# Performance work log

Measured on AMD Instinct MI355X. Metric: run time of the kernel, lower is better.

## Reference

```python
import jax, jax.numpy as jnp
import numpy as np

B, N, D, F = 16, 64, 32, 32  # batch, nodes, node_dim, nb_features


def setup_inputs() -> dict:
    key = jax.random.key(0)
    k1, k2, k3, k4, k5 = jax.random.split(key, 5)
    nodes = jax.random.normal(k1, (B, N, D), dtype=jnp.float32)
    edges = jax.random.normal(k2, (B, N * N, F), dtype=jnp.float32)
    mask = jax.random.randint(k3, (B, N * N, 1), 0, 2).astype(jnp.float32)
    # Linear(nb_features -> node_dim**2) params, torch-style fan-in scaling
    lim = 1.0 / np.sqrt(F)
    W = jax.random.uniform(k4, (D * D, F), dtype=jnp.float32, minval=-lim, maxval=lim)
    b = jax.random.uniform(k5, (D * D,), dtype=jnp.float32, minval=-lim, maxval=lim)
    return {"nodes": nodes, "edges": edges, "mask": mask, "W": W, "b": b}


def reference(nodes, edges, mask, W, b):
    Bn, Nn, d = nodes.shape
    # ECC weight generation: per-edge d x d matrix from edge features
    A = jax.nn.relu(jnp.einsum('bef,gf->beg', edges, W) + b)      # [B, N*N, d*d]
    A = A.reshape(Bn, Nn, Nn, d, d)                               # [B, i, j, d, d]
    # node_j tiling: flat edge index i*N+j pairs with source node j
    messages = jnp.einsum('bijde,bje->bijd', A, nodes)            # [B, i, j, d]
    masked = messages * mask.reshape(Bn, Nn, Nn, 1)
    agg_m = jnp.sum(masked, axis=2)                               # [B, N, d]
    return agg_m
```

## Files before the change

kernel.cpp:

```cpp
#include <hip/hip_runtime.h>
#include <hip/hip_bf16.h>


#define B_ 16
#define N_ 64
#define D_ 32
#define F_ 32
#define NP 33

typedef __attribute__((ext_vector_type(8))) short bf16x8;
typedef __attribute__((ext_vector_type(4))) float f32x4;

__device__ __forceinline__ short f2bf(float x) {
    unsigned u = __builtin_bit_cast(unsigned, x);
    u += 0x7fffu + ((u >> 16) & 1u);
    return (short)(u >> 16);
}

__global__ __launch_bounds__(256) void ecc_fused_kernel(
    const float* __restrict__ nodes,
    const float* __restrict__ edges,
    const float* __restrict__ mask,
    const float* __restrict__ W,
    const float* __restrict__ bias,
    float* __restrict__ out)
{
    __shared__ short wlds[512 * F_];
    __shared__ float nmask[N_ * NP];
    __shared__ float blds[D_ * D_];

    const int tid  = threadIdx.x;
    const int lane = tid & 63;
    const int wv   = tid >> 6;
    const int col  = lane & 15;
    const int grp  = lane >> 4;
    const int bi   = blockIdx.x;
    const int b    = bi >> 6;
    const int i    = bi & 63;
    const int f0   = grp * 8;

    {
        const int j  = tid >> 2;
        const int c0 = (tid & 3) * 8;
        const float mk = mask[b * (N_ * N_) + i * N_ + j];
        const float* np = nodes + (b * N_ + j) * D_ + c0;
        f32x4 v0 = *(const f32x4*)np;
        f32x4 v1 = *(const f32x4*)(np + 4);
        float* dst = &nmask[j * NP + c0];
        dst[0] = v0[0] * mk; dst[1] = v0[1] * mk;
        dst[2] = v0[2] * mk; dst[3] = v0[3] * mk;
        dst[4] = v1[0] * mk; dst[5] = v1[1] * mk;
        dst[6] = v1[2] * mk; dst[7] = v1[3] * mk;
        *(f32x4*)(blds + tid * 4) = *(const f32x4*)(bias + tid * 4);
    }

    const float* eb = edges + (b * (N_ * N_) + i * N_) * F_;
    bf16x8 bfrag[4];
#pragma unroll
    for (int jt = 0; jt < 4; ++jt) {
        const float* s = eb + (jt * 16 + col) * F_ + f0;
        f32x4 e0 = *(const f32x4*)s;
        f32x4 e1 = *(const f32x4*)(s + 4);
        bf16x8 t;
        t[0] = f2bf(e0[0]); t[1] = f2bf(e0[1]); t[2] = f2bf(e0[2]); t[3] = f2bf(e0[3]);
        t[4] = f2bf(e1[0]); t[5] = f2bf(e1[1]); t[6] = f2bf(e1[2]); t[7] = f2bf(e1[3]);
        bfrag[jt] = t;
    }

    float acc[8] = {0.f, 0.f, 0.f, 0.f, 0.f, 0.f, 0.f, 0.f};

#pragma unroll 1
    for (int par = 0; par < 2; ++par) {
        __syncthreads();

#pragma unroll 2
        for (int k = 0; k < 8; ++k) {
            const int lidx = k * 2048 + tid * 8;
            const int lr   = lidx >> 5;
            const int fo   = lidx & 31;
            const int g    = (((lr >> 4) * 2 + par) * 16) + (lr & 15);
            const float* s = W + g * F_ + fo;
            f32x4 a0 = *(const f32x4*)s;
            f32x4 a1 = *(const f32x4*)(s + 4);
            bf16x8 t;
            t[0] = f2bf(a0[0]); t[1] = f2bf(a0[1]);
            t[2] = f2bf(a0[2]); t[3] = f2bf(a0[3]);
            t[4] = f2bf(a1[0]); t[5] = f2bf(a1[1]);
            t[6] = f2bf(a1[2]); t[7] = f2bf(a1[3]);
            *(bf16x8*)(wlds + lidx) = t;
        }
        __syncthreads();

        float nd[4][4];
#pragma unroll
        for (int jt = 0; jt < 4; ++jt) {
            const float* n = &nmask[(jt * 16 + col) * NP + par * 16 + grp * 4];
            nd[jt][0] = n[0]; nd[jt][1] = n[1];
            nd[jt][2] = n[2]; nd[jt][3] = n[3];
        }

#pragma unroll 1
        for (int g8 = 0; g8 < 8; ++g8) {
            const int gt   = wv * 16 + g8 * 2 + par;
            const int lrow = (wv * 8 + g8) * 16 + col;
            bf16x8 afrag = *(const bf16x8*)(wlds + lrow * F_ + f0);
            f32x4 bfr = *(const f32x4*)(blds + gt * 16 + grp * 4);

#pragma unroll
            for (int jt = 0; jt < 4; ++jt) {
                f32x4 c = __builtin_amdgcn_mfma_f32_16x16x32_bf16(afrag, bfrag[jt], bfr, 0, 0, 0);
                float s = fmaxf(c[0], 0.f) * nd[jt][0];
                s += fmaxf(c[1], 0.f) * nd[jt][1];
                s += fmaxf(c[2], 0.f) * nd[jt][2];
                s += fmaxf(c[3], 0.f) * nd[jt][3];
                acc[g8] += s;
            }
        }
    }

#pragma unroll
    for (int dl = 0; dl < 8; ++dl) {
        float v = acc[dl];
#pragma unroll
        for (int off = 32; off > 0; off >>= 1) v += __shfl_xor(v, off, 64);
        acc[dl] = v;
    }

    if (lane == 0) {
        float* op = out + (b * N_ + i) * D_ + wv * 8;
#pragma unroll
        for (int dl = 0; dl < 8; ++dl) op[dl] = acc[dl];
    }
}

extern "C" void kernel_launch(void* const* d_in, const int* in_sizes, int n_in,
                              void* d_out, int out_size, void* d_ws, size_t ws_size,
                              hipStream_t stream) {
    const float* nodes = (const float*)d_in[0];
    const float* edges = (const float*)d_in[1];
    const float* mask  = (const float*)d_in[2];
    const float* W     = (const float*)d_in[3];
    const float* bias  = (const float*)d_in[4];
    float* outp        = (float*)d_out;

    ecc_fused_kernel<<<dim3(B_ * N_), dim3(256), 0, stream>>>(
        nodes, edges, mask, W, bias, outp);
}
```

Measured before the change: 86.75 us.

## Compact masked edges per row and load full swizzled W tile once

Builds a compacted list of unmasked source nodes per (batch, row) with a ballot and popcount, then gathers only those edges and node vectors and skips MFMA tiles past the active count. The whole bf16 W matrix is staged into LDS once with an XOR swizzle instead of twice per parity pass, which removes a barrier pair and reduces bank conflicts. This uses 64KB of LDS, which may lower occupancy, and adds a data-dependent branch on the tile count. Since the mask is random, about half the MFMA work is skipped.

Measured after the change: 92.72 us. +6.9%, slower.

```diff
diff --git a/kernel.cpp b/kernel.cpp
--- a/kernel.cpp
+++ b/kernel.cpp
@@ -25,9 +25,11 @@
     const float* __restrict__ bias,
     float* __restrict__ out)
 {
-    __shared__ short wlds[512 * F_];
+    __shared__ short wlds[D_ * D_ * F_];
     __shared__ float nmask[N_ * NP];
     __shared__ float blds[D_ * D_];
+    __shared__ int   jlist[N_];
+    __shared__ int   jcnt;
 
     const int tid  = threadIdx.x;
     const int lane = tid & 63;
@@ -39,81 +41,102 @@
     const int i    = bi & 63;
     const int f0   = grp * 8;
 
+    *(f32x4*)(blds + tid * 4) = *(const f32x4*)(bias + tid * 4);
+
+    if (tid < 64) {
+        const float mk = mask[b * (N_ * N_) + i * N_ + tid];
+        jlist[tid] = 0;
+        const unsigned long long act = __ballot(mk != 0.0f);
+        if (tid == 0) jcnt = (int)__popcll(act);
+        if (mk != 0.0f) {
+            const int pos = (int)__popcll(act & ((1ull << tid) - 1ull));
+            jlist[pos] = tid;
+        }
+    }
+
+#pragma unroll 1
+    for (int k = 0; k < 16; ++k) {
+        const int lidx = k * 2048 + tid * 8;
+        const int lr   = lidx >> 5;
+        const int fo   = lidx & 31;
+        const float* s = W + lr * F_ + fo;
+        f32x4 a0 = *(const f32x4*)s;
+        f32x4 a1 = *(const f32x4*)(s + 4);
+        bf16x8 t;
+        t[0] = f2bf(a0[0]); t[1] = f2bf(a0[1]);
+        t[2] = f2bf(a0[2]); t[3] = f2bf(a0[3]);
+        t[4] = f2bf(a1[0]); t[5] = f2bf(a1[1]);
+        t[6] = f2bf(a1[2]); t[7] = f2bf(a1[3]);
+        *(bf16x8*)(wlds + lr * F_ + (fo ^ ((lr & 3) * 8))) = t;
+    }
+    __syncthreads();
+
     {
-        const int j  = tid >> 2;
-        const int c0 = (tid & 3) * 8;
-        const float mk = mask[b * (N_ * N_) + i * N_ + j];
-        const float* np = nodes + (b * N_ + j) * D_ + c0;
-        f32x4 v0 = *(const f32x4*)np;
-        f32x4 v1 = *(const f32x4*)(np + 4);
-        float* dst = &nmask[j * NP + c0];
-        dst[0] = v0[0] * mk; dst[1] = v0[1] * mk;
-        dst[2] = v0[2] * mk; dst[3] = v0[3] * mk;
-        dst[4] = v1[0] * mk; dst[5] = v1[1] * mk;
-        dst[6] = v1[2] * mk; dst[7] = v1[3] * mk;
-        *(f32x4*)(blds + tid * 4) = *(const f32x4*)(bias + tid * 4);
+        const int slot = tid >> 2;
+        const int c0   = (tid & 3) * 8;
+        f32x4 v0 = {0.f, 0.f, 0.f, 0.f}, v1 = {0.f, 0.f, 0.f, 0.f};
+        if (slot < jcnt) {
+            const float* np = nodes + (b * N_ + jlist[slot]) * D_ + c0;
+            v0 = *(const f32x4*)np;
+            v1 = *(const f32x4*)(np + 4);
+        }
+        float* dst = &nmask[slot * NP + c0];
+        dst[0] = v0[0]; dst[1] = v0[1]; dst[2] = v0[2]; dst[3] = v0[3];
+        dst[4] = v1[0]; dst[5] = v1[1]; dst[6] = v1[2]; dst[7] = v1[3];
     }
+
+    const int NT = (jcnt + 15) >> 4;
 
     const float* eb = edges + (b * (N_ * N_) + i * N_) * F_;
     bf16x8 bfrag[4];
 #pragma unroll
     for (int jt = 0; jt < 4; ++jt) {
-        const float* s = eb + (jt * 16 + col) * F_ + f0;
-        f32x4 e0 = *(const f32x4*)s;
-        f32x4 e1 = *(const f32x4*)(s + 4);
-        bf16x8 t;
-        t[0] = f2bf(e0[0]); t[1] = f2bf(e0[1]); t[2] = f2bf(e0[2]); t[3] = f2bf(e0[3]);
-        t[4] = f2bf(e1[0]); t[5] = f2bf(e1[1]); t[6] = f2bf(e1[2]); t[7] = f2bf(e1[3]);
-        bfrag[jt] = t;
+        if (jt < NT) {
+            const int j = jlist[jt * 16 + col];
+            const float* s = eb + j * F_ + f0;
+            f32x4 e0 = *(const f32x4*)s;
+            f32x4 e1 = *(const f32x4*)(s + 4);
+            bf16x8 t;
+            t[0] = f2bf(e0[0]); t[1] = f2bf(e0[1]);
+            t[2] = f2bf(e0[2]); t[3] = f2bf(e0[3]);
+            t[4] = f2bf(e1[0]); t[5] = f2bf(e1[1]);
+            t[6] = f2bf(e1[2]); t[7] = f2bf(e1[3]);
+            bfrag[jt] = t;
+        }
     }
+    __syncthreads();
 
     float acc[8] = {0.f, 0.f, 0.f, 0.f, 0.f, 0.f, 0.f, 0.f};
 
 #pragma unroll 1
     for (int par = 0; par < 2; ++par) {
-        __syncthreads();
-
-#pragma unroll 2
-        for (int k = 0; k < 8; ++k) {
-            const int lidx = k * 2048 + tid * 8;
-            const int lr   = lidx >> 5;
-            const int fo   = lidx & 31;
-            const int g    = (((lr >> 4) * 2 + par) * 16) + (lr & 15);
-            const float* s = W + g * F_ + fo;
-            f32x4 a0 = *(const f32x4*)s;
-            f32x4 a1 = *(const f32x4*)(s + 4);
-            bf16x8 t;
-            t[0] = f2bf(a0[0]); t[1] = f2bf(a0[1]);
-            t[2] = f2bf(a0[2]); t[3] = f2bf(a0[3]);
-            t[4] = f2bf(a1[0]); t[5] = f2bf(a1[1]);
-            t[6] = f2bf(a1[2]); t[7] = f2bf(a1[3]);
-            *(bf16x8*)(wlds + lidx) = t;
-        }
-        __syncthreads();
-
         float nd[4][4];
 #pragma unroll
         for (int jt = 0; jt < 4; ++jt) {
-            const float* n = &nmask[(jt * 16 + col) * NP + par * 16 + grp * 4];
-            nd[jt][0] = n[0]; nd[jt][1] = n[1];
-            nd[jt][2] = n[2]; nd[jt][3] = n[3];
+            if (jt < NT) {
+                const float* n = &nmask[(jt * 16 + col) * NP + par * 16 + grp * 4];
+                nd[jt][0] = n[0]; nd[jt][1] = n[1];
+                nd[jt][2] = n[2]; nd[jt][3] = n[3];
+            }
         }
 
 #pragma unroll 1
         for (int g8 = 0; g8 < 8; ++g8) {
-            const int gt   = wv * 16 + g8 * 2 + par;
-            const int lrow = (wv * 8 + g8) * 16 + col;
-            bf16x8 afrag = *(const bf16x8*)(wlds + lrow * F_ + f0);
+            const int gt  = wv * 16 + g8 * 2 + par;
+            const int row = gt * 16 + col;
+            bf16x8 afrag = *(const bf16x8*)(wlds + row * F_ + ((grp ^ (row & 3)) * 8));
             f32x4 bfr = *(const f32x4*)(blds + gt * 16 + grp * 4);
 
 #pragma unroll
             for (int jt = 0; jt < 4; ++jt) {
-                f32x4 c = __builtin_amdgcn_mfma_f32_16x16x32_bf16(afrag, bfrag[jt], bfr, 0, 0, 0);
-                float s = fmaxf(c[0], 0.f) * nd[jt][0];
-                s += fmaxf(c[1], 0.f) * nd[jt][1];
-                s += fmaxf(c[2], 0.f) * nd[jt][2];
-                s += fmaxf(c[3], 0.f) * nd[jt][3];
-                acc[g8] += s;
+                if (jt < NT) {
+                    f32x4 c = __builtin_amdgcn_mfma_f32_16x16x32_bf16(afrag, bfrag[jt], bfr, 0, 0, 0);
+                    float s = fmaxf(c[0], 0.f) * nd[jt][0];
+                    s += fmaxf(c[1], 0.f) * nd[jt][1];
+                    s += fmaxf(c[2], 0.f) * nd[jt][2];
+                    s += fmaxf(c[3], 0.f) * nd[jt][3];
+                    acc[g8] += s;
+                }
             }
         }
     }
```
